# Optimization experiments

Measured on AMD Instinct MI355X. Metric: run time of the kernel, lower is better.

The kernel has to match this reference:

```python
import jax, jax.numpy as jnp
import numpy as np

N = 4096  # size of every layer (I, H1, H2, O)
EPS = 1e-5  # torch LayerNorm default


def _ln(x, g, b):
    # torch.nn.LayerNorm: biased variance, affine
    mu = jnp.mean(x)
    xc = x - mu
    v = jnp.mean(xc * xc)
    return xc * jax.lax.rsqrt(v + EPS) * g + b


def setup_inputs() -> dict:
    key = jax.random.key(0)
    ks = jax.random.split(key, 24)
    W = 0.02  # weight scale ~ uniform-init magnitude of nn.Linear at fan_in=4096
    inp = {
        "input_raw": jax.random.normal(ks[0], (N,), jnp.float32),
        "h1_prev": jax.random.normal(ks[1], (N,), jnp.float32),
        "h2_prev": jax.random.normal(ks[2], (N,), jnp.float32),
        "W_I_H1": jax.random.normal(ks[3], (N, N), jnp.float32) * W,
        "W_H1_H1": jax.random.normal(ks[4], (N, N), jnp.float32) * W,
        "W_H1_H2": jax.random.normal(ks[5], (N, N), jnp.float32) * W,
        "W_H2_H1": jax.random.normal(ks[6], (N, N), jnp.float32) * W,
        "W_H2_H2": jax.random.normal(ks[7], (N, N), jnp.float32) * W,
        "W_H1_O": jax.random.normal(ks[8], (N, N), jnp.float32) * W,
        "W_H2_O": jax.random.normal(ks[9], (N, N), jnp.float32) * W,
        "bias_h1": jax.random.normal(ks[10], (N,), jnp.float32) * 0.1,
        "bias_h2": jax.random.normal(ks[11], (N,), jnp.float32) * 0.1,
        "bias_o": jax.random.normal(ks[12], (N,), jnp.float32) * 0.1,
        "g_i": jax.random.uniform(ks[13], (N,), jnp.float32, 0.5, 1.5),
        "b_i": jax.random.normal(ks[14], (N,), jnp.float32) * 0.1,
        "g_h1": jax.random.uniform(ks[15], (N,), jnp.float32, 0.5, 1.5),
        "bln_h1": jax.random.normal(ks[16], (N,), jnp.float32) * 0.1,
        "g_h2": jax.random.uniform(ks[17], (N,), jnp.float32, 0.5, 1.5),
        "bln_h2": jax.random.normal(ks[18], (N,), jnp.float32) * 0.1,
        "g_o": jax.random.uniform(ks[19], (N,), jnp.float32, 0.5, 1.5),
        "bln_o": jax.random.normal(ks[20], (N,), jnp.float32) * 0.1,
    }
    return inp


def reference(input_raw, h1_prev, h2_prev,
              W_I_H1, W_H1_H1, W_H1_H2, W_H2_H1, W_H2_H2, W_H1_O, W_H2_O,
              bias_h1, bias_h2, bias_o,
              g_i, b_i, g_h1, bln_h1, g_h2, bln_h2, g_o, bln_o):
    # --- Phase 1: feedback accumulation + per-layer LayerNorm ---
    # I and O have no feedback -> LN(zeros) = LN bias (beta)
    i_out = b_i + input_raw                       # layers['I']: LN(0) then += input_raw
    h1_fb = _ln(W_H1_H1 @ h1_prev, g_h1, bln_h1)  # self-recurrent feedback H1->H1
    h2_fb = _ln(W_H2_H2 @ h2_prev, g_h2, bln_h2)  # self-recurrent feedback H2->H2
    o_init = bln_o                                # layers['O']: LN(zeros)

    # --- Phase 2: input-driven / feedback-only hidden activations ---
    h1_p2 = jax.nn.relu(_ln(W_I_H1 @ i_out + h1_fb + bias_h1, g_h1, bln_h1))  # 'I' in forward
    h2_p2 = jax.nn.relu(_ln(h2_fb + bias_h2, g_h2, bln_h2))                    # feedback-only

    # --- Phase 3: inter-hidden forward pass (intermediate_output OVERWRITES) ---
    h1_f = jax.nn.relu(_ln(W_H2_H1 @ h2_p2 + bias_h1, g_h1, bln_h1))
    h2_f = jax.nn.relu(_ln(W_H1_H2 @ h1_p2 + bias_h2, g_h2, bln_h2))

    # --- Output layer: sum forwards, tanh(LN(.)) ---
    o = jnp.tanh(_ln(o_init + W_H1_O @ h1_f + W_H2_O @ h2_f + bias_o, g_o, bln_o))
    return o
```

## Files before the change

### kernel.cpp

```cpp
#include <hip/hip_runtime.h>
#include <math.h>

#define NN 4096
#define ROWS_PER_BLOCK 16
#define BLK 256


__device__ __forceinline__ float4 ld4(const float* __restrict__ p, int t) {
    return reinterpret_cast<const float4*>(p)[t];
}
__device__ __forceinline__ void st4(float* __restrict__ p, int t, float4 v) {
    reinterpret_cast<float4*>(p)[t] = v;
}
__device__ __forceinline__ float4 add4(float4 a, float4 b) {
    return make_float4(a.x + b.x, a.y + b.y, a.z + b.z, a.w + b.w);
}

typedef const __attribute__((address_space(1))) unsigned int* gas1_u32;
typedef __attribute__((address_space(3))) unsigned int* las3_u32;
template<int AUX>
__device__ __forceinline__ void async16(const float* g, float* l) {
    __builtin_amdgcn_global_load_lds((gas1_u32)(const void*)g, (las3_u32)(void*)l, 16, 0, AUX);
}

template<int AUX>
__device__ __forceinline__ void stage_row(const float* __restrict__ W, int row,
                                          float* __restrict__ buf, int wave, int lane) {
    const float* g = W + (size_t)row * NN + wave * 1024 + lane * 4;
    float* l = buf + wave * 1024;
    async16<AUX>(g,       l);
    async16<AUX>(g + 256, l + 256);
    async16<AUX>(g + 512, l + 512);
    async16<AUX>(g + 768, l + 768);
}

__device__ __forceinline__ float dot_row(const float* __restrict__ buf,
                                         const float4 xr[4], int tid) {
    const float4* b4 = reinterpret_cast<const float4*>(buf);
    float p = 0.f;
    #pragma unroll
    for (int i = 0; i < 4; ++i) {
        float4 w = b4[i * 256 + tid];
        p = fmaf(w.x, xr[i].x, p);
        p = fmaf(w.y, xr[i].y, p);
        p = fmaf(w.z, xr[i].z, p);
        p = fmaf(w.w, xr[i].w, p);
    }
    #pragma unroll
    for (int off = 32; off > 0; off >>= 1) p += __shfl_down(p, off, 64);
    return p;
}

__device__ __forceinline__ float2 block_reduce2(float s, float ss, float* sbuf) {
    #pragma unroll
    for (int off = 32; off > 0; off >>= 1) {
        s  += __shfl_down(s,  off, 64);
        ss += __shfl_down(ss, off, 64);
    }
    const int wave = threadIdx.x >> 6;
    const int lane = threadIdx.x & 63;
    if (lane == 0) { sbuf[wave] = s; sbuf[16 + wave] = ss; }
    __syncthreads();
    float rs = 0.f, rss = 0.f;
    if (threadIdx.x < 16) { rs = sbuf[threadIdx.x]; rss = sbuf[16 + threadIdx.x]; }
    if (wave == 0) {
        #pragma unroll
        for (int off = 8; off > 0; off >>= 1) {
            rs  += __shfl_down(rs,  off, 64);
            rss += __shfl_down(rss, off, 64);
        }
        if (lane == 0) { sbuf[0] = rs; sbuf[1] = rss; }
    }
    __syncthreads();
    float2 r = make_float2(sbuf[0], sbuf[1]);
    __syncthreads();
    return r;
}

struct LNStat { float mu, rstd; };

__device__ __forceinline__ LNStat ln_stats(float4 v, float* sbuf) {
    float s  = v.x + v.y + v.z + v.w;
    float ss = v.x * v.x + v.y * v.y + v.z * v.z + v.w * v.w;
    float2 r = block_reduce2(s, ss, sbuf);
    LNStat o;
    o.mu = r.x * (1.0f / NN);
    float var = r.y * (1.0f / NN) - o.mu * o.mu;
    o.rstd = rsqrtf(var + 1e-5f);
    return o;
}

__device__ __forceinline__ float4 ln_apply(float4 v, LNStat st, float4 g, float4 b) {
    return make_float4((v.x - st.mu) * st.rstd * g.x + b.x,
                       (v.y - st.mu) * st.rstd * g.y + b.y,
                       (v.z - st.mu) * st.rstd * g.z + b.z,
                       (v.w - st.mu) * st.rstd * g.w + b.w);
}

__device__ __forceinline__ float4 relu4(float4 v) {
    return make_float4(fmaxf(v.x, 0.f), fmaxf(v.y, 0.f), fmaxf(v.z, 0.f), fmaxf(v.w, 0.f));
}


template<int AUX>
__device__ __forceinline__ void gemv_core(const float* __restrict__ W,
                                          const float* __restrict__ x,
                                          const float* __restrict__ xadd,
                                          float* __restrict__ y,
                                          float* t0, float* t1, float* sbuf) {
    const int tid  = threadIdx.x;
    const int wave = tid >> 6;
    const int lane = tid & 63;
    const int r0 = blockIdx.x * ROWS_PER_BLOCK;

    stage_row<AUX>(W, r0, t0, wave, lane);

    float4 xr[4];
    const float4* x4 = reinterpret_cast<const float4*>(x);
    #pragma unroll
    for (int i = 0; i < 4; ++i) xr[i] = x4[i * 256 + tid];
    if (xadd) {
        const float4* a4 = reinterpret_cast<const float4*>(xadd);
        #pragma unroll
        for (int i = 0; i < 4; ++i) xr[i] = add4(xr[i], a4[i * 256 + tid]);
    }
    __syncthreads();

    #pragma unroll 1
    for (int j = 0; j < ROWS_PER_BLOCK; j += 2) {
        if (tid == 0 && j > 0) y[r0 + j - 1] = sbuf[4] + sbuf[5] + sbuf[6] + sbuf[7];
        if (j + 1 < ROWS_PER_BLOCK) stage_row<AUX>(W, r0 + j + 1, t1, wave, lane);
        {
            float p = dot_row(t0, xr, tid);
            if (lane == 0) sbuf[wave] = p;
        }
        __syncthreads();
        if (tid == 0) y[r0 + j] = sbuf[0] + sbuf[1] + sbuf[2] + sbuf[3];
        if (j + 2 < ROWS_PER_BLOCK) stage_row<AUX>(W, r0 + j + 2, t0, wave, lane);
        {
            float p = dot_row(t1, xr, tid);
            if (lane == 0) sbuf[4 + wave] = p;
        }
        __syncthreads();
    }
    if (tid == 0) y[r0 + ROWS_PER_BLOCK - 1] = sbuf[4] + sbuf[5] + sbuf[6] + sbuf[7];
}

__global__ __launch_bounds__(BLK) void gemv_stageA(
    const float* __restrict__ W_H1_H1, const float* __restrict__ h1_prev,
    const float* __restrict__ W_H2_H2, const float* __restrict__ h2_prev,
    const float* __restrict__ W_I_H1,  const float* __restrict__ input_raw,
    const float* __restrict__ b_i,
    float* __restrict__ mv1, float* __restrict__ mv2, float* __restrict__ mv3)
{
    __shared__ float t0[NN], t1[NN];
    __shared__ float sbuf[8];
    const float* W; const float* x; const float* xadd; float* y;
    if (blockIdx.y == 0)      { W = W_H1_H1; x = h1_prev;   xadd = nullptr; y = mv1; }
    else if (blockIdx.y == 1) { W = W_H2_H2; x = h2_prev;   xadd = nullptr; y = mv2; }
    else                      { W = W_I_H1;  x = input_raw; xadd = b_i;     y = mv3; }
    gemv_core<2>(W, x, xadd, y, t0, t1, sbuf);
}

__global__ __launch_bounds__(BLK) void gemv_pair(
    const float* __restrict__ Wa, const float* __restrict__ xa, float* __restrict__ ya,
    const float* __restrict__ Wb, const float* __restrict__ xb, float* __restrict__ yb)
{
    __shared__ float t0[NN], t1[NN];
    __shared__ float sbuf[8];
    const float* W; const float* x; float* y;
    if (blockIdx.y == 0) { W = Wa; x = xa; y = ya; }
    else                 { W = Wb; x = xb; y = yb; }
    gemv_core<0>(W, x, nullptr, y, t0, t1, sbuf);
}

__global__ __launch_bounds__(1024) void phase2_kernel(
    const float* __restrict__ mv1, const float* __restrict__ mv2, const float* __restrict__ mv3,
    const float* __restrict__ bias_h1, const float* __restrict__ bias_h2,
    const float* __restrict__ g_h1, const float* __restrict__ bln_h1,
    const float* __restrict__ g_h2, const float* __restrict__ bln_h2,
    float* __restrict__ h1_p2, float* __restrict__ h2_p2)
{
    __shared__ float sbuf[32];
    const int t = threadIdx.x;
    if (blockIdx.x == 0) {
        float4 g = ld4(g_h1, t), b = ld4(bln_h1, t);
        float4 v = ld4(mv1, t);
        LNStat s1 = ln_stats(v, sbuf);
        float4 fb = ln_apply(v, s1, g, b);
        float4 tt = add4(add4(ld4(mv3, t), fb), ld4(bias_h1, t));
        LNStat s2 = ln_stats(tt, sbuf);
        st4(h1_p2, t, relu4(ln_apply(tt, s2, g, b)));
    } else {
        float4 g = ld4(g_h2, t), b = ld4(bln_h2, t);
        float4 v = ld4(mv2, t);
        LNStat s1 = ln_stats(v, sbuf);
        float4 fb = ln_apply(v, s1, g, b);
        float4 tt = add4(fb, ld4(bias_h2, t));
        LNStat s2 = ln_stats(tt, sbuf);
        st4(h2_p2, t, relu4(ln_apply(tt, s2, g, b)));
    }
}

__global__ __launch_bounds__(1024) void phase3_kernel(
    const float* __restrict__ mv4, const float* __restrict__ mv5,
    const float* __restrict__ bias_h1, const float* __restrict__ bias_h2,
    const float* __restrict__ g_h1, const float* __restrict__ bln_h1,
    const float* __restrict__ g_h2, const float* __restrict__ bln_h2,
    float* __restrict__ h1_f, float* __restrict__ h2_f)
{
    __shared__ float sbuf[32];
    const int t = threadIdx.x;
    const float* mv;  const float* bias; const float* g; const float* b; float* out;
    if (blockIdx.x == 0) { mv = mv4; bias = bias_h1; g = g_h1; b = bln_h1; out = h1_f; }
    else                 { mv = mv5; bias = bias_h2; g = g_h2; b = bln_h2; out = h2_f; }
    float4 v = add4(ld4(mv, t), ld4(bias, t));
    LNStat s = ln_stats(v, sbuf);
    st4(out, t, relu4(ln_apply(v, s, ld4(g, t), ld4(b, t))));
}

__global__ __launch_bounds__(1024) void final_kernel(
    const float* __restrict__ mv6, const float* __restrict__ mv7,
    const float* __restrict__ bias_o, const float* __restrict__ bln_o,
    const float* __restrict__ g_o,
    float* __restrict__ out)
{
    __shared__ float sbuf[32];
    const int t = threadIdx.x;
    float4 v = add4(add4(ld4(bln_o, t), ld4(mv6, t)), add4(ld4(mv7, t), ld4(bias_o, t)));
    LNStat s = ln_stats(v, sbuf);
    float4 r = ln_apply(v, s, ld4(g_o, t), ld4(bln_o, t));
    st4(out, t, make_float4(tanhf(r.x), tanhf(r.y), tanhf(r.z), tanhf(r.w)));
}


extern "C" void kernel_launch(void* const* d_in, const int* in_sizes, int n_in,
                              void* d_out, int out_size, void* d_ws, size_t ws_size,
                              hipStream_t stream) {
    const float* input_raw = (const float*)d_in[0];
    const float* h1_prev   = (const float*)d_in[1];
    const float* h2_prev   = (const float*)d_in[2];
    const float* W_I_H1    = (const float*)d_in[3];
    const float* W_H1_H1   = (const float*)d_in[4];
    const float* W_H1_H2   = (const float*)d_in[5];
    const float* W_H2_H1   = (const float*)d_in[6];
    const float* W_H2_H2   = (const float*)d_in[7];
    const float* W_H1_O    = (const float*)d_in[8];
    const float* W_H2_O    = (const float*)d_in[9];
    const float* bias_h1   = (const float*)d_in[10];
    const float* bias_h2   = (const float*)d_in[11];
    const float* bias_o    = (const float*)d_in[12];
    const float* b_i       = (const float*)d_in[14];
    const float* g_h1      = (const float*)d_in[15];
    const float* bln_h1    = (const float*)d_in[16];
    const float* g_h2      = (const float*)d_in[17];
    const float* bln_h2    = (const float*)d_in[18];
    const float* g_o       = (const float*)d_in[19];
    const float* bln_o     = (const float*)d_in[20];

    float* ws    = (float*)d_ws;
    float* mv1   = ws;
    float* mv2   = ws + 1 * NN;
    float* mv3   = ws + 2 * NN;
    float* h1_p2 = ws + 3 * NN;
    float* h2_p2 = ws + 4 * NN;
    float* mv4   = ws + 5 * NN;
    float* mv5   = ws + 6 * NN;
    float* h1_f  = ws + 7 * NN;
    float* h2_f  = ws + 8 * NN;
    float* mv6   = ws + 9 * NN;
    float* mv7   = ws + 10 * NN;

    const int gx = NN / ROWS_PER_BLOCK;

    gemv_stageA<<<dim3(gx, 3), BLK, 0, stream>>>(
        W_H1_H1, h1_prev, W_H2_H2, h2_prev, W_I_H1, input_raw, b_i, mv1, mv2, mv3);

    phase2_kernel<<<2, 1024, 0, stream>>>(
        mv1, mv2, mv3, bias_h1, bias_h2, g_h1, bln_h1, g_h2, bln_h2, h1_p2, h2_p2);

    gemv_pair<<<dim3(gx, 2), BLK, 0, stream>>>(
        W_H2_H1, h2_p2, mv4, W_H1_H2, h1_p2, mv5);

    phase3_kernel<<<2, 1024, 0, stream>>>(
        mv4, mv5, bias_h1, bias_h2, g_h1, bln_h1, g_h2, bln_h2, h1_f, h2_f);

    gemv_pair<<<dim3(gx, 2), BLK, 0, stream>>>(
        W_H1_O, h1_f, mv6, W_H2_O, h2_f, mv7);

    final_kernel<<<1, 1024, 0, stream>>>(
        mv6, mv7, bias_o, bln_o, g_o, (float*)d_out);
}
```

Baseline: 89.69 us.

## Fuse LayerNorm epilogues into GEMV kernels via last-block atomic counter

Removes the three separate small LayerNorm kernels by having the last block to finish each GEMV (detected with an atomic counter plus threadfence) run the LayerNorm/activation epilogue with 256 threads over 4096 elements. This cuts three kernel launches and their inter-kernel gaps but adds a memset launch. The cost is that the epilogue now runs on a single 256-thread block serially after the GEMV, instead of on one or two 1024-thread blocks.

```diff
diff --git a/kernel.cpp b/kernel.cpp
--- a/kernel.cpp
+++ b/kernel.cpp
@@ -51,7 +51,15 @@
     return p;
 }
 
-__device__ __forceinline__ float2 block_reduce2(float s, float ss, float* sbuf) {
+struct LNStat { float mu, rstd; };
+
+__device__ __forceinline__ LNStat stats256(const float4 v[4], float* rbuf) {
+    float s = 0.f, ss = 0.f;
+    #pragma unroll
+    for (int i = 0; i < 4; ++i) {
+        s  += v[i].x + v[i].y + v[i].z + v[i].w;
+        ss += v[i].x * v[i].x + v[i].y * v[i].y + v[i].z * v[i].z + v[i].w * v[i].w;
+    }
     #pragma unroll
     for (int off = 32; off > 0; off >>= 1) {
         s  += __shfl_down(s,  off, 64);
@@ -59,34 +67,18 @@
     }
     const int wave = threadIdx.x >> 6;
     const int lane = threadIdx.x & 63;
-    if (lane == 0) { sbuf[wave] = s; sbuf[16 + wave] = ss; }
-    __syncthreads();
-    float rs = 0.f, rss = 0.f;
-    if (threadIdx.x < 16) { rs = sbuf[threadIdx.x]; rss = sbuf[16 + threadIdx.x]; }
-    if (wave == 0) {
-        #pragma unroll
-        for (int off = 8; off > 0; off >>= 1) {
-            rs  += __shfl_down(rs,  off, 64);
-            rss += __shfl_down(rss, off, 64);
-        }
-        if (lane == 0) { sbuf[0] = rs; sbuf[1] = rss; }
-    }
-    __syncthreads();
-    float2 r = make_float2(sbuf[0], sbuf[1]);
-    __syncthreads();
-    return r;
-}
-
-struct LNStat { float mu, rstd; };
-
-__device__ __forceinline__ LNStat ln_stats(float4 v, float* sbuf) {
-    float s  = v.x + v.y + v.z + v.w;
-    float ss = v.x * v.x + v.y * v.y + v.z * v.z + v.w * v.w;
-    float2 r = block_reduce2(s, ss, sbuf);
+    if (lane == 0) { rbuf[wave] = s; rbuf[4 + wave] = ss; }
+    __syncthreads();
+    if (threadIdx.x == 0) {
+        rbuf[8] = rbuf[0] + rbuf[1] + rbuf[2] + rbuf[3];
+        rbuf[9] = rbuf[4] + rbuf[5] + rbuf[6] + rbuf[7];
+    }
+    __syncthreads();
     LNStat o;
-    o.mu = r.x * (1.0f / NN);
-    float var = r.y * (1.0f / NN) - o.mu * o.mu;
+    o.mu = rbuf[8] * (1.0f / NN);
+    float var = rbuf[9] * (1.0f / NN) - o.mu * o.mu;
     o.rstd = rsqrtf(var + 1e-5f);
+    __syncthreads();
     return o;
 }
 
@@ -146,91 +138,147 @@
     if (tid == 0) y[r0 + ROWS_PER_BLOCK - 1] = sbuf[4] + sbuf[5] + sbuf[6] + sbuf[7];
 }
 
+__device__ __forceinline__ bool last_block(int* counter, int total, int* flagbuf) {
+    if (threadIdx.x == 0) {
+        __threadfence();
+        int old = atomicAdd(counter, 1);
+        *flagbuf = (old == total - 1);
+    }
+    __syncthreads();
+    bool last = (*flagbuf != 0);
+    if (last) __threadfence();
+    return last;
+}
+
 __global__ __launch_bounds__(BLK) void gemv_stageA(
     const float* __restrict__ W_H1_H1, const float* __restrict__ h1_prev,
     const float* __restrict__ W_H2_H2, const float* __restrict__ h2_prev,
     const float* __restrict__ W_I_H1,  const float* __restrict__ input_raw,
     const float* __restrict__ b_i,
-    float* __restrict__ mv1, float* __restrict__ mv2, float* __restrict__ mv3)
+    float* __restrict__ mv1, float* __restrict__ mv2, float* __restrict__ mv3,
+    const float* __restrict__ bias_h1, const float* __restrict__ bias_h2,
+    const float* __restrict__ g_h1, const float* __restrict__ bln_h1,
+    const float* __restrict__ g_h2, const float* __restrict__ bln_h2,
+    float* __restrict__ h1_p2, float* __restrict__ h2_p2,
+    int* __restrict__ counter)
 {
     __shared__ float t0[NN], t1[NN];
-    __shared__ float sbuf[8];
+    __shared__ float sbuf[16];
+    __shared__ int   flagbuf;
     const float* W; const float* x; const float* xadd; float* y;
     if (blockIdx.y == 0)      { W = W_H1_H1; x = h1_prev;   xadd = nullptr; y = mv1; }
     else if (blockIdx.y == 1) { W = W_H2_H2; x = h2_prev;   xadd = nullptr; y = mv2; }
     else                      { W = W_I_H1;  x = input_raw; xadd = b_i;     y = mv3; }
     gemv_core<2>(W, x, xadd, y, t0, t1, sbuf);
-}
-
-__global__ __launch_bounds__(BLK) void gemv_pair(
-    const float* __restrict__ Wa, const float* __restrict__ xa, float* __restrict__ ya,
-    const float* __restrict__ Wb, const float* __restrict__ xb, float* __restrict__ yb)
-{
-    __shared__ float t0[NN], t1[NN];
-    __shared__ float sbuf[8];
-    const float* W; const float* x; float* y;
-    if (blockIdx.y == 0) { W = Wa; x = xa; y = ya; }
-    else                 { W = Wb; x = xb; y = yb; }
-    gemv_core<0>(W, x, nullptr, y, t0, t1, sbuf);
-}
-
-__global__ __launch_bounds__(1024) void phase2_kernel(
-    const float* __restrict__ mv1, const float* __restrict__ mv2, const float* __restrict__ mv3,
+
+    if (!last_block(counter, 3 * (NN / ROWS_PER_BLOCK), &flagbuf)) return;
+
+    const int t = threadIdx.x;
+    float4 g[4], b[4], v[4];
+    #pragma unroll
+    for (int i = 0; i < 4; ++i) {
+        const int j = i * 256 + t;
+        g[i] = ld4(g_h1, j); b[i] = ld4(bln_h1, j); v[i] = ld4(mv1, j);
+    }
+    LNStat s = stats256(v, sbuf);
+    #pragma unroll
+    for (int i = 0; i < 4; ++i) {
+        const int j = i * 256 + t;
+        v[i] = add4(add4(ld4(mv3, j), ln_apply(v[i], s, g[i], b[i])), ld4(bias_h1, j));
+    }
+    s = stats256(v, sbuf);
+    #pragma unroll
+    for (int i = 0; i < 4; ++i) st4(h1_p2, i * 256 + t, relu4(ln_apply(v[i], s, g[i], b[i])));
+    #pragma unroll
+    for (int i = 0; i < 4; ++i) {
+        const int j = i * 256 + t;
+        g[i] = ld4(g_h2, j); b[i] = ld4(bln_h2, j); v[i] = ld4(mv2, j);
+    }
+    s = stats256(v, sbuf);
+    #pragma unroll
+    for (int i = 0; i < 4; ++i)
+        v[i] = add4(ln_apply(v[i], s, g[i], b[i]), ld4(bias_h2, i * 256 + t));
+    s = stats256(v, sbuf);
+    #pragma unroll
+    for (int i = 0; i < 4; ++i) st4(h2_p2, i * 256 + t, relu4(ln_apply(v[i], s, g[i], b[i])));
+}
+
+__global__ __launch_bounds__(BLK) void gemv_stageB(
+    const float* __restrict__ W_H2_H1, const float* __restrict__ h2_p2,
+    const float* __restrict__ W_H1_H2, const float* __restrict__ h1_p2,
+    float* __restrict__ mv4, float* __restrict__ mv5,
     const float* __restrict__ bias_h1, const float* __restrict__ bias_h2,
     const float* __restrict__ g_h1, const float* __restrict__ bln_h1,
     const float* __restrict__ g_h2, const float* __restrict__ bln_h2,
-    float* __restrict__ h1_p2, float* __restrict__ h2_p2)
+    float* __restrict__ h1_f, float* __restrict__ h2_f,
+    int* __restrict__ counter)
 {
-    __shared__ float sbuf[32];
+    __shared__ float t0[NN], t1[NN];
+    __shared__ float sbuf[16];
+    __shared__ int   flagbuf;
+    const float* W; const float* x; float* y;
+    if (blockIdx.y == 0) { W = W_H2_H1; x = h2_p2; y = mv4; }
+    else                 { W = W_H1_H2; x = h1_p2; y = mv5; }
+    gemv_core<0>(W, x, nullptr, y, t0, t1, sbuf);
+
+    if (!last_block(counter, 2 * (NN / ROWS_PER_BLOCK), &flagbuf)) return;
+
     const int t = threadIdx.x;
-    if (blockIdx.x == 0) {
-        float4 g = ld4(g_h1, t), b = ld4(bln_h1, t);
-        float4 v = ld4(mv1, t);
-        LNStat s1 = ln_stats(v, sbuf);
-        float4 fb = ln_apply(v, s1, g, b);
-        float4 tt = add4(add4(ld4(mv3, t), fb), ld4(bias_h1, t));
-        LNStat s2 = ln_stats(tt, sbuf);
-        st4(h1_p2, t, relu4(ln_apply(tt, s2, g, b)));
-    } else {
-        float4 g = ld4(g_h2, t), b = ld4(bln_h2, t);
-        float4 v = ld4(mv2, t);
-        LNStat s1 = ln_stats(v, sbuf);
-        float4 fb = ln_apply(v, s1, g, b);
-        float4 tt = add4(fb, ld4(bias_h2, t));
-        LNStat s2 = ln_stats(tt, sbuf);
-        st4(h2_p2, t, relu4(ln_apply(tt, s2, g, b)));
-    }
-}
-
-__global__ __launch_bounds__(1024) void phase3_kernel(
-    const float* __restrict__ mv4, const float* __restrict__ mv5,
-    const float* __restrict__ bias_h1, const float* __restrict__ bias_h2,
-    const float* __restrict__ g_h1, const float* __restrict__ bln_h1,
-    const float* __restrict__ g_h2, const float* __restrict__ bln_h2,
-    float* __restrict__ h1_f, float* __restrict__ h2_f)
-{
-    __shared__ float sbuf[32];
-    const int t = threadIdx.x;
-    const float* mv;  const float* bias; const float* g; const float* b; float* out;
-    if (blockIdx.x == 0) { mv = mv4; bias = bias_h1; g = g_h1; b = bln_h1; out = h1_f; }
-    else                 { mv = mv5; bias = bias_h2; g = g_h2; b = bln_h2; out = h2_f; }
-    float4 v = add4(ld4(mv, t), ld4(bias, t));
-    LNStat s = ln_stats(v, sbuf);
-    st4(out, t, relu4(ln_apply(v, s, ld4(g, t), ld4(b, t))));
-}
-
-__global__ __launch_bounds__(1024) void final_kernel(
-    const float* __restrict__ mv6, const float* __restrict__ mv7,
+    float4 g[4], b[4], v[4];
+    #pragma unroll
+    for (int i = 0; i < 4; ++i) {
+        const int j = i * 256 + t;
+        g[i] = ld4(g_h1, j); b[i] = ld4(bln_h1, j);
+        v[i] = add4(ld4(mv4, j), ld4(bias_h1, j));
+    }
+    LNStat s = stats256(v, sbuf);
+    #pragma unroll
+    for (int i = 0; i < 4; ++i) st4(h1_f, i * 256 + t, relu4(ln_apply(v[i], s, g[i], b[i])));
+    #pragma unroll
+    for (int i = 0; i < 4; ++i) {
+        const int j = i * 256 + t;
+        g[i] = ld4(g_h2, j); b[i] = ld4(bln_h2, j);
+        v[i] = add4(ld4(mv5, j), ld4(bias_h2, j));
+    }
+    s = stats256(v, sbuf);
+    #pragma unroll
+    for (int i = 0; i < 4; ++i) st4(h2_f, i * 256 + t, relu4(ln_apply(v[i], s, g[i], b[i])));
+}
+
+__global__ __launch_bounds__(BLK) void gemv_stageC(
+    const float* __restrict__ W_H1_O, const float* __restrict__ h1_f,
+    const float* __restrict__ W_H2_O, const float* __restrict__ h2_f,
+    float* __restrict__ mv6, float* __restrict__ mv7,
     const float* __restrict__ bias_o, const float* __restrict__ bln_o,
     const float* __restrict__ g_o,
-    float* __restrict__ out)
+    float* __restrict__ out,
+    int* __restrict__ counter)
 {
-    __shared__ float sbuf[32];
+    __shared__ float t0[NN], t1[NN];
+    __shared__ float sbuf[16];
+    __shared__ int   flagbuf;
+    const float* W; const float* x; float* y;
+    if (blockIdx.y == 0) { W = W_H1_O; x = h1_f; y = mv6; }
+    else                 { W = W_H2_O; x = h2_f; y = mv7; }
+    gemv_core<0>(W, x, nullptr, y, t0, t1, sbuf);
+
+    if (!last_block(counter, 2 * (NN / ROWS_PER_BLOCK), &flagbuf)) return;
+
     const int t = threadIdx.x;
-    float4 v = add4(add4(ld4(bln_o, t), ld4(mv6, t)), add4(ld4(mv7, t), ld4(bias_o, t)));
-    LNStat s = ln_stats(v, sbuf);
-    float4 r = ln_apply(v, s, ld4(g_o, t), ld4(bln_o, t));
-    st4(out, t, make_float4(tanhf(r.x), tanhf(r.y), tanhf(r.z), tanhf(r.w)));
+    float4 g[4], b[4], v[4];
+    #pragma unroll
+    for (int i = 0; i < 4; ++i) {
+        const int j = i * 256 + t;
+        g[i] = ld4(g_o, j); b[i] = ld4(bln_o, j);
+        v[i] = add4(add4(b[i], ld4(mv6, j)), add4(ld4(mv7, j), ld4(bias_o, j)));
+    }
+    LNStat s = stats256(v, sbuf);
+    #pragma unroll
+    for (int i = 0; i < 4; ++i) {
+        float4 r = ln_apply(v[i], s, g[i], b[i]);
+        st4(out, i * 256 + t,
+            make_float4(tanhf(r.x), tanhf(r.y), tanhf(r.z), tanhf(r.w)));
+    }
 }
 
 
@@ -270,24 +318,23 @@
     float* h2_f  = ws + 8 * NN;
     float* mv6   = ws + 9 * NN;
     float* mv7   = ws + 10 * NN;
+    int*   counters = (int*)(ws + 12 * NN);
+
+    hipMemsetAsync(counters, 0, 3 * sizeof(int), stream);
 
     const int gx = NN / ROWS_PER_BLOCK;
 
     gemv_stageA<<<dim3(gx, 3), BLK, 0, stream>>>(
-        W_H1_H1, h1_prev, W_H2_H2, h2_prev, W_I_H1, input_raw, b_i, mv1, mv2, mv3);
-
-    phase2_kernel<<<2, 1024, 0, stream>>>(
-        mv1, mv2, mv3, bias_h1, bias_h2, g_h1, bln_h1, g_h2, bln_h2, h1_p2, h2_p2);
-
-    gemv_pair<<<dim3(gx, 2), BLK, 0, stream>>>(
-        W_H2_H1, h2_p2, mv4, W_H1_H2, h1_p2, mv5);
-
-    phase3_kernel<<<2, 1024, 0, stream>>>(
-        mv4, mv5, bias_h1, bias_h2, g_h1, bln_h1, g_h2, bln_h2, h1_f, h2_f);
-
-    gemv_pair<<<dim3(gx, 2), BLK, 0, stream>>>(
-        W_H1_O, h1_f, mv6, W_H2_O, h2_f, mv7);
-
-    final_kernel<<<1, 1024, 0, stream>>>(
-        mv6, mv7, bias_o, bln_o, g_o, (float*)d_out);
-}
+        W_H1_H1, h1_prev, W_H2_H2, h2_prev, W_I_H1, input_raw, b_i,
+        mv1, mv2, mv3, bias_h1, bias_h2, g_h1, bln_h1, g_h2, bln_h2,
+        h1_p2, h2_p2, counters + 0);
+
+    gemv_stageB<<<dim3(gx, 2), BLK, 0, stream>>>(
+        W_H2_H1, h2_p2, W_H1_H2, h1_p2, mv4, mv5,
+        bias_h1, bias_h2, g_h1, bln_h1, g_h2, bln_h2,
+        h1_f, h2_f, counters + 1);
+
+    gemv_stageC<<<dim3(gx, 2), BLK, 0, stream>>>(
+        W_H1_O, h1_f, W_H2_O, h2_f, mv6, mv7,
+        bias_o, bln_o, g_o, (float*)d_out, counters + 2);
+}
```

After: 152.7 us. +70.2%, slower.
